# Kernel tuning notes

Measured on AMD Instinct MI355X. Metric: run time of the kernel, lower is better.

Reference implementation:

```python
import jax, jax.numpy as jnp
import numpy as np

NUM_EMBEDDINGS = 1024
EMBEDDING_DIM = 64
COMMITMENT_COST = 0.25


def setup_inputs() -> dict:
    key = jax.random.key(0)
    k1, k2 = jax.random.split(key)
    inputs = jax.random.normal(k1, (64, 32, 32, EMBEDDING_DIM), dtype=jnp.float32)
    # torch init is uniform(-1/K, 1/K); scale accordingly
    weight = jax.random.uniform(
        k2, (NUM_EMBEDDINGS, EMBEDDING_DIM), dtype=jnp.float32,
        minval=-1.0 / NUM_EMBEDDINGS, maxval=1.0 / NUM_EMBEDDINGS)
    return {"inputs": inputs, "weight": weight}


def reference(inputs, weight):
    input_shape = inputs.shape
    flat = inputs.reshape(-1, EMBEDDING_DIM)               # [N, D]
    distances = (jnp.sum(flat ** 2, axis=1, keepdims=True)
                 + jnp.sum(weight ** 2, axis=1)
                 - 2.0 * flat @ weight.T)                   # [N, K]
    encoding_indices = jnp.argmin(distances, axis=1)        # [N]
    # gather codes (equivalent to one-hot @ weight, but as a direct gather)
    quantized = weight[encoding_indices].reshape(input_shape)

    e_latent_loss = jnp.mean((jax.lax.stop_gradient(quantized) - inputs) ** 2)
    q_latent_loss = jnp.mean((quantized - jax.lax.stop_gradient(inputs)) ** 2)
    loss = q_latent_loss + COMMITMENT_COST * e_latent_loss

    # straight-through estimator
    quantized_ste = inputs + jax.lax.stop_gradient(quantized - inputs)

    # perplexity (equivalent to mean over the one-hot encodings)
    n_tokens = flat.shape[0]
    counts = jax.ops.segment_sum(
        jnp.ones((n_tokens,), jnp.float32), encoding_indices,
        num_segments=NUM_EMBEDDINGS)
    avg_probs = counts / n_tokens
    perplexity = jnp.exp(-jnp.sum(avg_probs * jnp.log(avg_probs + 1e-10)))

    indices_for_transformer = encoding_indices.reshape(input_shape[0], -1)
    return (loss, quantized_ste, perplexity, indices_for_transformer)
```

## Files before the change

### kernel.cpp

```cpp
#include <hip/hip_runtime.h>
#include <cstdint>
#include <cstddef>

#define N_TOKENS 65536
#define DIM 64
#define K_CODES 1024
#define NTH 256
#define TPB 256
#define NCH 16
#define NBLK (N_TOKENS / TPB)

#define OFF_Q 1
#define OFF_PERP 4194305
#define OFF_IDX 4194306

#define MARGIN 2.5e-5f
#define XSCALE 1024.0f
#define WSCALE 65536.0f
#define AINIT_SC -33554432.0f
#define D_UNSC  -2.9802322387695312e-08f

#define WS_LOSS   0
#define WS_TICKET 8
#define WS_COUNTS 16
#define WS_WHI    4112
#define WS_WLO    135184
#define WS_S2     266256

typedef _Float16 f16x8 __attribute__((ext_vector_type(8)));
typedef float    f32x4 __attribute__((ext_vector_type(4)));

__device__ __forceinline__ float fmulr(float a, float b){ return __fmul_rn(a,b); }
__device__ __forceinline__ float faddr(float a, float b){ return __fadd_rn(a,b); }

__device__ __forceinline__ unsigned keyf(float f) {
    unsigned u = __float_as_uint(f);
    return u ^ ((u & 0x80000000u) ? 0xffffffffu : 0x80000000u);
}

__device__ __forceinline__ void split16(float v, _Float16& h, _Float16& l) {
    h = (_Float16)v;
    l = (_Float16)(v - (float)h);
}

__device__ float sumsq64_np(const float* __restrict__ p) {
    float s[16];
    #pragma unroll
    for (int l = 0; l < 16; ++l) {
        float a0 = fmulr(p[l],      p[l]);
        float a1 = fmulr(p[l + 16], p[l + 16]);
        float a2 = fmulr(p[l + 32], p[l + 32]);
        float a3 = fmulr(p[l + 48], p[l + 48]);
        s[l] = faddr(faddr(a0, a1), faddr(a2, a3));
    }
    #pragma unroll
    for (int len = 8; len >= 1; len >>= 1)
        #pragma unroll
        for (int l = 0; l < len; ++l)
            s[l] = faddr(s[l], s[l + len]);
    return s[0];
}

__device__ __forceinline__ void async_copy16(const void* g, void* l) {
    __builtin_amdgcn_global_load_lds(
        (const __attribute__((address_space(1))) void*)g,
        (__attribute__((address_space(3))) void*)l, 16, 0, 0);
}

__global__ void vq_prep(const float* __restrict__ W, _Float16* __restrict__ Whi,
                        _Float16* __restrict__ Wlo, float* __restrict__ s2g,
                        int* __restrict__ counts, int* __restrict__ ticket,
                        double* __restrict__ loss_acc) {
    int gid = blockIdx.x * NTH + threadIdx.x;
    for (int e = gid; e < K_CODES * DIM; e += 16384) {
        float vs = W[e] * WSCALE;
        _Float16 h, l; split16(vs, h, l);
        int j = e >> 6, k = e & 63;
        int pos = j * 64 + (((k >> 3) ^ (j & 7)) << 3) + (k & 7);
        Whi[pos] = h; Wlo[pos] = l;
    }
    if (gid < K_CODES) { s2g[gid] = sumsq64_np(W + gid * 64); counts[gid] = 0; }
    if (gid == 0) { *loss_acc = 0.0; *ticket = 0; }
}

__global__ __launch_bounds__(NTH, 1)
void vq_main(const float* __restrict__ X, const float* __restrict__ W,
             const _Float16* __restrict__ WhiG, const _Float16* __restrict__ WloG,
             const float* __restrict__ s2g, float* __restrict__ out,
             double* __restrict__ loss_acc, int* __restrict__ counts,
             int* __restrict__ ticket) {
    __shared__ __align__(16) _Float16 xs_hi[TPB * 64];
    __shared__ __align__(16) _Float16 xs_lo[TPB * 64];
    __shared__ __align__(16) _Float16 ws_hi[2][64 * 64];
    __shared__ __align__(16) _Float16 ws_lo[2][64 * 64];
    __shared__ __align__(16) float s2s[K_CODES];
    __shared__ int fidx[TPB];
    __shared__ int flist[TPB];
    __shared__ int fcount, lastFlag;
    __shared__ double lred[4];

    const int tid  = threadIdx.x;
    const int lane = tid & 63, wave = tid >> 6;
    const int quad = lane >> 4, lrow = lane & 15;
    const int t0   = blockIdx.x * TPB;

    if (tid == 0) fcount = 0;

    {
        const char* gh = (const char*)WhiG;
        const char* gl = (const char*)WloG;
        char* lh = (char*)&ws_hi[0][0] + wave * 1024;
        char* ll = (char*)&ws_lo[0][0] + wave * 1024;
        #pragma unroll
        for (int i = 0; i < 2; ++i) {
            async_copy16(gh + i * 4096 + tid * 16, lh + i * 4096);
            async_copy16(gl + i * 4096 + tid * 16, ll + i * 4096);
        }
    }
    *(f32x4*)&s2s[tid * 4] = *(const f32x4*)&s2g[tid * 4];
    #pragma unroll
    for (int i = 0; i < 8; ++i) {
        int g = tid + NTH * i;
        int t = g >> 3, kb = g & 7;
        const float* src = X + (size_t)(t0 + t) * DIM + kb * 8;
        float v[8];
        *(f32x4*)v       = *(const f32x4*)src;
        *(f32x4*)(v + 4) = *(const f32x4*)(src + 4);
        _Float16 h[8], l[8];
        #pragma unroll
        for (int k = 0; k < 8; ++k) split16(v[k] * XSCALE, h[k], l[k]);
        int base = t * 64 + ((kb ^ (t & 7)) << 3);
        *(f16x8*)&xs_hi[base] = *(f16x8*)h;
        *(f16x8*)&xs_lo[base] = *(f16x8*)l;
    }
    __syncthreads();

    f16x8 a_h0[4], a_h1[4], a_l0[4], a_l1[4];
    #pragma unroll
    for (int rt = 0; rt < 4; ++rt) {
        int tf = wave * 64 + rt * 16 + lrow;
        int sA = tf & 7;
        a_h0[rt] = *(const f16x8*)&xs_hi[tf * 64 + (((0 + quad) ^ sA) << 3)];
        a_h1[rt] = *(const f16x8*)&xs_hi[tf * 64 + (((4 + quad) ^ sA) << 3)];
        a_l0[rt] = *(const f16x8*)&xs_lo[tf * 64 + (((0 + quad) ^ sA) << 3)];
        a_l1[rt] = *(const f16x8*)&xs_lo[tf * 64 + (((4 + quad) ^ sA) << 3)];
    }

    float r1v[16], r2v[16]; int r1i[16];
    #pragma unroll
    for (int ri = 0; ri < 16; ++ri) { r1v[ri] = 3.4e38f; r2v[ri] = 3.4e38f; r1i[ri] = 0x7fffffff; }

    for (int ch = 0; ch < NCH; ++ch) {
        const int buf = ch & 1;
        if (ch < NCH - 1) {
            const char* gh = (const char*)WhiG + (ch + 1) * 8192;
            const char* gl = (const char*)WloG + (ch + 1) * 8192;
            char* lh = (char*)&ws_hi[buf ^ 1][0] + wave * 1024;
            char* ll = (char*)&ws_lo[buf ^ 1][0] + wave * 1024;
            #pragma unroll
            for (int i = 0; i < 2; ++i) {
                async_copy16(gh + i * 4096 + tid * 16, lh + i * 4096);
                async_copy16(gl + i * 4096 + tid * 16, ll + i * 4096);
            }
        }
        #pragma unroll
        for (int ct = 0; ct < 4; ++ct) {
            int lc = ct * 16 + lrow;
            int sB = lrow & 7;
            const _Float16* bh = &ws_hi[buf][lc * 64];
            const _Float16* bl = &ws_lo[buf][lc * 64];
            f16x8 b_h0 = *(const f16x8*)&bh[((0 + quad) ^ sB) << 3];
            f16x8 b_h1 = *(const f16x8*)&bh[((4 + quad) ^ sB) << 3];
            f16x8 b_l0 = *(const f16x8*)&bl[((0 + quad) ^ sB) << 3];
            f16x8 b_l1 = *(const f16x8*)&bl[((4 + quad) ^ sB) << 3];
            int jcode = ch * 64 + lc;
            float ainit = fmulr(s2s[jcode], AINIT_SC);
            #pragma unroll
            for (int rt = 0; rt < 4; ++rt) {
                f32x4 acc = {ainit, ainit, ainit, ainit};
                acc = __builtin_amdgcn_mfma_f32_16x16x32_f16(a_h0[rt], b_h0, acc, 0, 0, 0);
                acc = __builtin_amdgcn_mfma_f32_16x16x32_f16(a_h1[rt], b_h1, acc, 0, 0, 0);
                acc = __builtin_amdgcn_mfma_f32_16x16x32_f16(a_h0[rt], b_l0, acc, 0, 0, 0);
                acc = __builtin_amdgcn_mfma_f32_16x16x32_f16(a_h1[rt], b_l1, acc, 0, 0, 0);
                acc = __builtin_amdgcn_mfma_f32_16x16x32_f16(a_l0[rt], b_h0, acc, 0, 0, 0);
                acc = __builtin_amdgcn_mfma_f32_16x16x32_f16(a_l1[rt], b_h1, acc, 0, 0, 0);
                #pragma unroll
                for (int r = 0; r < 4; ++r) {
                    float d = fmulr(acc[r], D_UNSC);
                    int ri = rt * 4 + r;
                    bool lt = d < r1v[ri];
                    float sec = lt ? r1v[ri] : d;
                    r2v[ri] = fminf(r2v[ri], sec);
                    r1v[ri] = lt ? d : r1v[ri];
                    r1i[ri] = lt ? jcode : r1i[ri];
                }
            }
        }
        __syncthreads();
    }

    #pragma unroll
    for (int m = 1; m <= 8; m <<= 1) {
        #pragma unroll
        for (int ri = 0; ri < 16; ++ri) {
            float o1v = __shfl_xor(r1v[ri], m, 64);
            int   o1i = __shfl_xor(r1i[ri], m, 64);
            float o2v = __shfl_xor(r2v[ri], m, 64);
            bool take = (o1v < r1v[ri]) || (o1v == r1v[ri] && o1i < r1i[ri]);
            float loser = take ? r1v[ri] : o1v;
            r2v[ri] = fminf(fminf(r2v[ri], o2v), loser);
            if (take) { r1v[ri] = o1v; r1i[ri] = o1i; }
        }
    }
    if (lrow == 0) {
        #pragma unroll
        for (int ri = 0; ri < 16; ++ri) {
            int rt = ri >> 2, r = ri & 3;
            int t = wave * 64 + rt * 16 + quad * 4 + r;
            bool fb = (r2v[ri] - r1v[ri]) < MARGIN;
            fidx[t] = fb ? (r1i[ri] | (int)0x80000000) : r1i[ri];
            if (fb) { int p = atomicAdd(&fcount, 1); flist[p] = t; }
        }
    }
    __syncthreads();

    double lsum = 0.0;
    #pragma unroll
    for (int i = 0; i < 16; ++i) {
        int e4 = tid + NTH * i;
        int t = e4 >> 4, d4 = (e4 & 15) * 4;
        int iv = fidx[t];
        if (iv >= 0) {
            f32x4 q = *(const f32x4*)&W[iv * 64 + d4];
            f32x4 x = *(const f32x4*)&X[(size_t)(t0 + t) * 64 + d4];
            *(f32x4*)&out[(size_t)OFF_Q + (size_t)(t0 + t) * 64 + d4] = q;
            #pragma unroll
            for (int c = 0; c < 4; ++c) {
                float df = __fsub_rn(q[c], x[c]);
                lsum += (double)fmulr(df, df);
            }
        }
    }
    #pragma unroll
    for (int off = 32; off >= 1; off >>= 1) lsum += __shfl_down(lsum, off, 64);
    if (lane == 0) lred[wave] = lsum;
    if (tid < TPB) {
        int iv = fidx[tid];
        if (iv >= 0) {
            atomicAdd(&counts[iv], 1);
            out[(size_t)OFF_IDX + t0 + tid] = (float)iv;
        }
    }
    __syncthreads();
    if (tid == 0) atomicAdd(loss_acc, lred[0] + lred[1] + lred[2] + lred[3]);

    for (int fi = wave; fi < fcount; fi += 4) {
        int t = flist[fi];
        int gtok = t0 + t;
        float s1v = sumsq64_np(X + (size_t)gtok * 64);
        f32x4 xr[16];
        #pragma unroll
        for (int kb = 0; kb < 16; ++kb)
            xr[kb] = *(const f32x4*)(X + (size_t)gtok * 64 + kb * 4);
        unsigned long long best = ~0ULL;
        #pragma unroll 1
        for (int c16 = 0; c16 < 16; ++c16) {
            int code = lane * 16 + c16;
            const float* wr = W + code * 64;
            float acc = 0.0f;
            #pragma unroll
            for (int kb = 0; kb < 16; ++kb) {
                f32x4 wv = *(const f32x4*)(wr + kb * 4);
                acc = __builtin_fmaf(xr[kb][0], wv[0], acc);
                acc = __builtin_fmaf(xr[kb][1], wv[1], acc);
                acc = __builtin_fmaf(xr[kb][2], wv[2], acc);
                acc = __builtin_fmaf(xr[kb][3], wv[3], acc);
            }
            float d = faddr(faddr(s1v, s2s[code]), fmulr(-2.0f, acc));
            unsigned long long pk = ((unsigned long long)keyf(d) << 32) | (unsigned)code;
            best = pk < best ? pk : best;
        }
        #pragma unroll
        for (int m = 32; m >= 1; m >>= 1) {
            unsigned long long o = __shfl_xor(best, m, 64);
            best = o < best ? o : best;
        }
        int idx = (int)(best & 0xffffffffu);
        float q = W[idx * 64 + lane];
        float x = X[(size_t)gtok * 64 + lane];
        out[(size_t)OFF_Q + (size_t)gtok * 64 + lane] = q;
        float df = __fsub_rn(q, x);
        double ls = (double)fmulr(df, df);
        #pragma unroll
        for (int m = 32; m >= 1; m >>= 1) ls += __shfl_xor(ls, m, 64);
        if (lane == 0) {
            out[(size_t)OFF_IDX + gtok] = (float)idx;
            atomicAdd(&counts[idx], 1);
            atomicAdd(loss_acc, ls);
        }
    }

    __syncthreads();
    if (tid == 0) {
        __threadfence();
        int old = atomicAdd(ticket, 1);
        lastFlag = (old == NBLK - 1) ? 1 : 0;
    }
    __syncthreads();
    if (lastFlag) {
        double h = 0.0;
        for (int j = tid; j < K_CODES; j += NTH) {
            int c = atomicAdd(&counts[j], 0);
            double p = (double)c / 65536.0;
            h += p * log(p + 1e-10);
        }
        #pragma unroll
        for (int off = 32; off >= 1; off >>= 1) h += __shfl_down(h, off, 64);
        if (lane == 0) lred[wave] = h;
        __syncthreads();
        if (tid == 0) {
            double H = lred[0] + lred[1] + lred[2] + lred[3];
            out[OFF_PERP] = (float)exp(-H);
            double ls = atomicAdd(loss_acc, 0.0);
            float Lf = (float)(ls / 4194304.0);
            out[0] = faddr(Lf, fmulr(0.25f, Lf));
        }
    }
}

extern "C" void kernel_launch(void* const* d_in, const int* in_sizes, int n_in,
                              void* d_out, int out_size, void* d_ws, size_t ws_size,
                              hipStream_t stream) {
    const float* X = (const float*)d_in[0];
    const float* W = (const float*)d_in[1];
    float* out = (float*)d_out;
    char* ws = (char*)d_ws;
    double* loss_acc = (double*)(ws + WS_LOSS);
    int* ticket = (int*)(ws + WS_TICKET);
    int* counts = (int*)(ws + WS_COUNTS);
    _Float16* Whi = (_Float16*)(ws + WS_WHI);
    _Float16* Wlo = (_Float16*)(ws + WS_WLO);
    float* s2g = (float*)(ws + WS_S2);

    vq_prep<<<64, NTH, 0, stream>>>(W, Whi, Wlo, s2g, counts, ticket, loss_acc);
    vq_main<<<NBLK, NTH, 0, stream>>>(X, W, Whi, Wlo, s2g, out,
                                      loss_acc, counts, ticket);
}
```

Measured before the change: 204.8 us.

## Drop LDS staging, split codebook across wave pairs with register-loaded operands

The main kernel no longer stages X and the codebook halves in shared memory with async copies and per-chunk barriers. Each wave now loads its X fragments and its codebook fragments straight from global memory into registers, with a register double buffer for B. Blocks cover 128 tokens, and two waves split the 1024 codes per token group, merging top-2 results through shared memory. The prep kernel is vectorised and drops the swizzle, and launch bounds allow two blocks per CU. This removes the barriers and LDS traffic and raises occupancy, but relies on L1/L2 for codebook reuse and doubles the number of blocks that reload it.

```diff
diff --git a/kernel.cpp b/kernel.cpp
--- a/kernel.cpp
+++ b/kernel.cpp
@@ -6,8 +6,7 @@
 #define DIM 64
 #define K_CODES 1024
 #define NTH 256
-#define TPB 256
-#define NCH 16
+#define TPB 128
 #define NBLK (N_TOKENS / TPB)
 
 #define OFF_Q 1
@@ -28,6 +27,7 @@
 #define WS_S2     266256
 
 typedef _Float16 f16x8 __attribute__((ext_vector_type(8)));
+typedef _Float16 f16x4 __attribute__((ext_vector_type(4)));
 typedef float    f32x4 __attribute__((ext_vector_type(4)));
 
 __device__ __forceinline__ float fmulr(float a, float b){ return __fmul_rn(a,b); }
@@ -61,142 +61,114 @@
     return s[0];
 }
 
-__device__ __forceinline__ void async_copy16(const void* g, void* l) {
-    __builtin_amdgcn_global_load_lds(
-        (const __attribute__((address_space(1))) void*)g,
-        (__attribute__((address_space(3))) void*)l, 16, 0, 0);
-}
-
 __global__ void vq_prep(const float* __restrict__ W, _Float16* __restrict__ Whi,
                         _Float16* __restrict__ Wlo, float* __restrict__ s2g,
                         int* __restrict__ counts, int* __restrict__ ticket,
                         double* __restrict__ loss_acc) {
     int gid = blockIdx.x * NTH + threadIdx.x;
-    for (int e = gid; e < K_CODES * DIM; e += 16384) {
-        float vs = W[e] * WSCALE;
-        _Float16 h, l; split16(vs, h, l);
-        int j = e >> 6, k = e & 63;
-        int pos = j * 64 + (((k >> 3) ^ (j & 7)) << 3) + (k & 7);
-        Whi[pos] = h; Wlo[pos] = l;
+    if (gid < 16384) {
+        f32x4 v = *(const f32x4*)(W + gid * 4);
+        f16x4 h, l;
+        #pragma unroll
+        for (int j = 0; j < 4; ++j) {
+            _Float16 hh, ll; split16(v[j] * WSCALE, hh, ll);
+            h[j] = hh; l[j] = ll;
+        }
+        *(f16x4*)(Whi + gid * 4) = h;
+        *(f16x4*)(Wlo + gid * 4) = l;
     }
     if (gid < K_CODES) { s2g[gid] = sumsq64_np(W + gid * 64); counts[gid] = 0; }
     if (gid == 0) { *loss_acc = 0.0; *ticket = 0; }
 }
 
-__global__ __launch_bounds__(NTH, 1)
+__global__ __launch_bounds__(NTH, 2)
 void vq_main(const float* __restrict__ X, const float* __restrict__ W,
              const _Float16* __restrict__ WhiG, const _Float16* __restrict__ WloG,
              const float* __restrict__ s2g, float* __restrict__ out,
              double* __restrict__ loss_acc, int* __restrict__ counts,
              int* __restrict__ ticket) {
-    __shared__ __align__(16) _Float16 xs_hi[TPB * 64];
-    __shared__ __align__(16) _Float16 xs_lo[TPB * 64];
-    __shared__ __align__(16) _Float16 ws_hi[2][64 * 64];
-    __shared__ __align__(16) _Float16 ws_lo[2][64 * 64];
-    __shared__ __align__(16) float s2s[K_CODES];
-    __shared__ int fidx[TPB];
-    __shared__ int flist[TPB];
-    __shared__ int fcount, lastFlag;
+    __shared__ float m1v[2][TPB];
+    __shared__ int   m1i[2][TPB];
+    __shared__ float m2v[2][TPB];
+    __shared__ int   fidx[TPB];
+    __shared__ int   flist[TPB];
+    __shared__ int   fcount, lastFlag;
     __shared__ double lred[4];
 
     const int tid  = threadIdx.x;
     const int lane = tid & 63, wave = tid >> 6;
     const int quad = lane >> 4, lrow = lane & 15;
     const int t0   = blockIdx.x * TPB;
+    const int wtok = t0 + (wave >> 1) * 64;
+    const int c0   = (wave & 1) * 512;
+    const int half = wave & 1;
 
     if (tid == 0) fcount = 0;
 
+    f16x8 a_h0[4], a_h1[4], a_l0[4], a_l1[4];
+    #pragma unroll
+    for (int rt = 0; rt < 4; ++rt) {
+        const float* xrow = X + (size_t)(wtok + rt * 16 + lrow) * DIM;
+        f32x4 v0 = *(const f32x4*)(xrow + quad * 8);
+        f32x4 v1 = *(const f32x4*)(xrow + quad * 8 + 4);
+        f32x4 v2 = *(const f32x4*)(xrow + 32 + quad * 8);
+        f32x4 v3 = *(const f32x4*)(xrow + 32 + quad * 8 + 4);
+        #pragma unroll
+        for (int j = 0; j < 4; ++j) {
+            _Float16 h, l;
+            split16(v0[j] * XSCALE, h, l); a_h0[rt][j]     = h; a_l0[rt][j]     = l;
+            split16(v1[j] * XSCALE, h, l); a_h0[rt][j + 4] = h; a_l0[rt][j + 4] = l;
+            split16(v2[j] * XSCALE, h, l); a_h1[rt][j]     = h; a_l1[rt][j]     = l;
+            split16(v3[j] * XSCALE, h, l); a_h1[rt][j + 4] = h; a_l1[rt][j + 4] = l;
+        }
+    }
+
+    float r1v[16], r2v[16]; int r1i[16];
+    #pragma unroll
+    for (int ri = 0; ri < 16; ++ri) { r1v[ri] = 3.4e38f; r2v[ri] = 3.4e38f; r1i[ri] = 0x7fffffff; }
+
+    f16x8 bh0[2], bh1[2], bl0[2], bl1[2]; float s2v[2];
     {
-        const char* gh = (const char*)WhiG;
-        const char* gl = (const char*)WloG;
-        char* lh = (char*)&ws_hi[0][0] + wave * 1024;
-        char* ll = (char*)&ws_lo[0][0] + wave * 1024;
-        #pragma unroll
-        for (int i = 0; i < 2; ++i) {
-            async_copy16(gh + i * 4096 + tid * 16, lh + i * 4096);
-            async_copy16(gl + i * 4096 + tid * 16, ll + i * 4096);
-        }
-    }
-    *(f32x4*)&s2s[tid * 4] = *(const f32x4*)&s2g[tid * 4];
-    #pragma unroll
-    for (int i = 0; i < 8; ++i) {
-        int g = tid + NTH * i;
-        int t = g >> 3, kb = g & 7;
-        const float* src = X + (size_t)(t0 + t) * DIM + kb * 8;
-        float v[8];
-        *(f32x4*)v       = *(const f32x4*)src;
-        *(f32x4*)(v + 4) = *(const f32x4*)(src + 4);
-        _Float16 h[8], l[8];
-        #pragma unroll
-        for (int k = 0; k < 8; ++k) split16(v[k] * XSCALE, h[k], l[k]);
-        int base = t * 64 + ((kb ^ (t & 7)) << 3);
-        *(f16x8*)&xs_hi[base] = *(f16x8*)h;
-        *(f16x8*)&xs_lo[base] = *(f16x8*)l;
-    }
-    __syncthreads();
-
-    f16x8 a_h0[4], a_h1[4], a_l0[4], a_l1[4];
-    #pragma unroll
-    for (int rt = 0; rt < 4; ++rt) {
-        int tf = wave * 64 + rt * 16 + lrow;
-        int sA = tf & 7;
-        a_h0[rt] = *(const f16x8*)&xs_hi[tf * 64 + (((0 + quad) ^ sA) << 3)];
-        a_h1[rt] = *(const f16x8*)&xs_hi[tf * 64 + (((4 + quad) ^ sA) << 3)];
-        a_l0[rt] = *(const f16x8*)&xs_lo[tf * 64 + (((0 + quad) ^ sA) << 3)];
-        a_l1[rt] = *(const f16x8*)&xs_lo[tf * 64 + (((4 + quad) ^ sA) << 3)];
-    }
-
-    float r1v[16], r2v[16]; int r1i[16];
-    #pragma unroll
-    for (int ri = 0; ri < 16; ++ri) { r1v[ri] = 3.4e38f; r2v[ri] = 3.4e38f; r1i[ri] = 0x7fffffff; }
-
-    for (int ch = 0; ch < NCH; ++ch) {
-        const int buf = ch & 1;
-        if (ch < NCH - 1) {
-            const char* gh = (const char*)WhiG + (ch + 1) * 8192;
-            const char* gl = (const char*)WloG + (ch + 1) * 8192;
-            char* lh = (char*)&ws_hi[buf ^ 1][0] + wave * 1024;
-            char* ll = (char*)&ws_lo[buf ^ 1][0] + wave * 1024;
+        int code = c0 + lrow;
+        const _Float16* ph = WhiG + code * 64 + quad * 8;
+        const _Float16* pl = WloG + code * 64 + quad * 8;
+        bh0[0] = *(const f16x8*)ph; bh1[0] = *(const f16x8*)(ph + 32);
+        bl0[0] = *(const f16x8*)pl; bl1[0] = *(const f16x8*)(pl + 32);
+        s2v[0] = s2g[code];
+    }
+    #pragma unroll 2
+    for (int tile = 0; tile < 32; ++tile) {
+        const int cur = tile & 1;
+        if (tile < 31) {
+            int code = c0 + (tile + 1) * 16 + lrow;
+            const _Float16* ph = WhiG + code * 64 + quad * 8;
+            const _Float16* pl = WloG + code * 64 + quad * 8;
+            bh0[cur ^ 1] = *(const f16x8*)ph; bh1[cur ^ 1] = *(const f16x8*)(ph + 32);
+            bl0[cur ^ 1] = *(const f16x8*)pl; bl1[cur ^ 1] = *(const f16x8*)(pl + 32);
+            s2v[cur ^ 1] = s2g[code];
+        }
+        int jcode = c0 + tile * 16 + lrow;
+        float ainit = fmulr(s2v[cur], AINIT_SC);
+        #pragma unroll
+        for (int rt = 0; rt < 4; ++rt) {
+            f32x4 acc = {ainit, ainit, ainit, ainit};
+            acc = __builtin_amdgcn_mfma_f32_16x16x32_f16(a_h0[rt], bh0[cur], acc, 0, 0, 0);
+            acc = __builtin_amdgcn_mfma_f32_16x16x32_f16(a_h1[rt], bh1[cur], acc, 0, 0, 0);
+            acc = __builtin_amdgcn_mfma_f32_16x16x32_f16(a_h0[rt], bl0[cur], acc, 0, 0, 0);
+            acc = __builtin_amdgcn_mfma_f32_16x16x32_f16(a_h1[rt], bl1[cur], acc, 0, 0, 0);
+            acc = __builtin_amdgcn_mfma_f32_16x16x32_f16(a_l0[rt], bh0[cur], acc, 0, 0, 0);
+            acc = __builtin_amdgcn_mfma_f32_16x16x32_f16(a_l1[rt], bh1[cur], acc, 0, 0, 0);
             #pragma unroll
-            for (int i = 0; i < 2; ++i) {
-                async_copy16(gh + i * 4096 + tid * 16, lh + i * 4096);
-                async_copy16(gl + i * 4096 + tid * 16, ll + i * 4096);
+            for (int r = 0; r < 4; ++r) {
+                float d = fmulr(acc[r], D_UNSC);
+                int ri = rt * 4 + r;
+                bool lt = d < r1v[ri];
+                float sec = lt ? r1v[ri] : d;
+                r2v[ri] = fminf(r2v[ri], sec);
+                r1v[ri] = lt ? d : r1v[ri];
+                r1i[ri] = lt ? jcode : r1i[ri];
             }
         }
-        #pragma unroll
-        for (int ct = 0; ct < 4; ++ct) {
-            int lc = ct * 16 + lrow;
-            int sB = lrow & 7;
-            const _Float16* bh = &ws_hi[buf][lc * 64];
-            const _Float16* bl = &ws_lo[buf][lc * 64];
-            f16x8 b_h0 = *(const f16x8*)&bh[((0 + quad) ^ sB) << 3];
-            f16x8 b_h1 = *(const f16x8*)&bh[((4 + quad) ^ sB) << 3];
-            f16x8 b_l0 = *(const f16x8*)&bl[((0 + quad) ^ sB) << 3];
-            f16x8 b_l1 = *(const f16x8*)&bl[((4 + quad) ^ sB) << 3];
-            int jcode = ch * 64 + lc;
-            float ainit = fmulr(s2s[jcode], AINIT_SC);
-            #pragma unroll
-            for (int rt = 0; rt < 4; ++rt) {
-                f32x4 acc = {ainit, ainit, ainit, ainit};
-                acc = __builtin_amdgcn_mfma_f32_16x16x32_f16(a_h0[rt], b_h0, acc, 0, 0, 0);
-                acc = __builtin_amdgcn_mfma_f32_16x16x32_f16(a_h1[rt], b_h1, acc, 0, 0, 0);
-                acc = __builtin_amdgcn_mfma_f32_16x16x32_f16(a_h0[rt], b_l0, acc, 0, 0, 0);
-                acc = __builtin_amdgcn_mfma_f32_16x16x32_f16(a_h1[rt], b_l1, acc, 0, 0, 0);
-                acc = __builtin_amdgcn_mfma_f32_16x16x32_f16(a_l0[rt], b_h0, acc, 0, 0, 0);
-                acc = __builtin_amdgcn_mfma_f32_16x16x32_f16(a_l1[rt], b_h1, acc, 0, 0, 0);
-                #pragma unroll
-                for (int r = 0; r < 4; ++r) {
-                    float d = fmulr(acc[r], D_UNSC);
-                    int ri = rt * 4 + r;
-                    bool lt = d < r1v[ri];
-                    float sec = lt ? r1v[ri] : d;
-                    r2v[ri] = fminf(r2v[ri], sec);
-                    r1v[ri] = lt ? d : r1v[ri];
-                    r1i[ri] = lt ? jcode : r1i[ri];
-                }
-            }
-        }
-        __syncthreads();
     }
 
     #pragma unroll
@@ -216,17 +188,30 @@
         #pragma unroll
         for (int ri = 0; ri < 16; ++ri) {
             int rt = ri >> 2, r = ri & 3;
-            int t = wave * 64 + rt * 16 + quad * 4 + r;
-            bool fb = (r2v[ri] - r1v[ri]) < MARGIN;
-            fidx[t] = fb ? (r1i[ri] | (int)0x80000000) : r1i[ri];
-            if (fb) { int p = atomicAdd(&fcount, 1); flist[p] = t; }
-        }
+            int tloc = (wave >> 1) * 64 + rt * 16 + quad * 4 + r;
+            m1v[half][tloc] = r1v[ri];
+            m1i[half][tloc] = r1i[ri];
+            m2v[half][tloc] = r2v[ri];
+        }
+    }
+    __syncthreads();
+
+    if (tid < TPB) {
+        float v0 = m1v[0][tid], v1 = m1v[1][tid];
+        bool t1 = v1 < v0;
+        float b1v = t1 ? v1 : v0;
+        int   b1i = t1 ? m1i[1][tid] : m1i[0][tid];
+        float loser = t1 ? v0 : v1;
+        float b2v = fminf(fminf(m2v[0][tid], m2v[1][tid]), loser);
+        bool fb = (b2v - b1v) < MARGIN;
+        fidx[tid] = fb ? (b1i | (int)0x80000000) : b1i;
+        if (fb) { int p = atomicAdd(&fcount, 1); flist[p] = tid; }
     }
     __syncthreads();
 
     double lsum = 0.0;
     #pragma unroll
-    for (int i = 0; i < 16; ++i) {
+    for (int i = 0; i < 8; ++i) {
         int e4 = tid + NTH * i;
         int t = e4 >> 4, d4 = (e4 & 15) * 4;
         int iv = fidx[t];
@@ -276,7 +261,7 @@
                 acc = __builtin_fmaf(xr[kb][2], wv[2], acc);
                 acc = __builtin_fmaf(xr[kb][3], wv[3], acc);
             }
-            float d = faddr(faddr(s1v, s2s[code]), fmulr(-2.0f, acc));
+            float d = faddr(faddr(s1v, s2g[code]), fmulr(-2.0f, acc));
             unsigned long long pk = ((unsigned long long)keyf(d) << 32) | (unsigned)code;
             best = pk < best ? pk : best;
         }
@@ -342,7 +327,7 @@
     _Float16* Wlo = (_Float16*)(ws + WS_WLO);
     float* s2g = (float*)(ws + WS_S2);
 
-    vq_prep<<<64, NTH, 0, stream>>>(W, Whi, Wlo, s2g, counts, ticket, loss_acc);
+    vq_prep<<<128, NTH, 0, stream>>>(W, Whi, Wlo, s2g, counts, ticket, loss_acc);
     vq_main<<<NBLK, NTH, 0, stream>>>(X, W, Whi, Wlo, s2g, out,
                                       loss_acc, counts, ticket);
 }
```

Result: faster. 187.1 us (-8.6%).
